# Kernel optimization log

Measured on AMD Instinct MI355X. Metric: run time of the kernel, lower is better.

The kernel has to match this reference:

```python
import jax, jax.numpy as jnp
import numpy as np

N_EXPERTS = 32
NUM_EXP = 4  # 1 shared + 3 routed

def setup_inputs() -> dict:
    key = jax.random.key(0)
    ks = jax.random.split(key, 4)
    b, t, c, h = 2, 2048, 256, 1024
    x = jax.random.normal(ks[0], (b, t, c), dtype=jnp.float32)
    gate_W = jax.random.normal(ks[1], (c, N_EXPERTS - 1), dtype=jnp.float32) / np.sqrt(c)
    gate_b = jnp.zeros((N_EXPERTS - 1,), jnp.float32)
    expert_bias = jnp.zeros((N_EXPERTS - 1,), jnp.float32)
    W1 = jax.random.normal(ks[2], (N_EXPERTS, c, h), dtype=jnp.float32) / np.sqrt(c)
    b1 = jnp.zeros((N_EXPERTS, h), jnp.float32)
    W2 = jax.random.normal(ks[3], (N_EXPERTS, h, c), dtype=jnp.float32) / np.sqrt(h)
    b2 = jnp.zeros((N_EXPERTS, c), jnp.float32)
    return {"x": x, "gate_W": gate_W, "gate_b": gate_b, "expert_bias": expert_bias,
            "W1": W1, "b1": b1, "W2": W2, "b2": b2}

def reference(x, gate_W, gate_b, expert_bias, W1, b1, W2, b2):
    # Eval mode: dropout and UnitCenteredNoise are identity.
    b, t, c = x.shape
    xf = x.reshape(b * t, c)                       # [N, c]
    N = xf.shape[0]

    # --- Router: softmax gate over 31 routed experts, bias, top-(num_exp-1) ---
    gate_cont = jax.nn.softmax(xf @ gate_W + gate_b, axis=-1)   # [N, 31]
    biased = gate_cont + expert_bias
    vals, idx = jax.lax.top_k(biased, NUM_EXP - 1)              # [N, 3]
    vals = vals / jnp.sum(vals, axis=-1, keepdims=True)
    shared_w = jnp.full((N, 1), 1.0 / NUM_EXP, dtype=x.dtype)
    gate_vals = jnp.concatenate([shared_w, vals * (NUM_EXP - 1) / NUM_EXP], axis=-1)  # [N, 4]
    idx_full = jnp.concatenate([jnp.zeros_like(idx[:, :1]), idx + 1], axis=-1)        # [N, 4]

    # --- Dense compute of ALL experts (faithful to original) ---
    hid = jax.nn.gelu(jnp.einsum('nc,ech->enh', xf, W1) + b1[:, None, :])  # [E, N, h]
    expert_out = jnp.einsum('enh,ehc->enc', hid, W2) + b2[:, None, :]      # [E, N, c]

    # --- Scatter gate weights into dense [N, E] router matrix ---
    router_weights = jnp.zeros((N, N_EXPERTS), dtype=x.dtype)
    router_weights = router_weights.at[jnp.arange(N)[:, None], idx_full].add(gate_vals)

    # --- Masked weighted sum over experts ---
    out = jnp.einsum('enc,ne->nc', expert_out, router_weights)  # [N, c]
    return out.reshape(b, t, c), router_weights
```

## Files before the change

### kernel.cpp

```cpp
#include <hip/hip_runtime.h>
#include <hip/hip_bf16.h>

#define NTOK 4096
#define CDIM 256
#define HDIM 1024
#define NEXP 32
#define MT   64
#define LDX  264
#define TP   72
#define NCPY 8
#define SEG  512
#define DUMP 16384
#define SROWS (DUMP + 1)

typedef __bf16 bf16x8 __attribute__((ext_vector_type(8)));
typedef float  f32x4  __attribute__((ext_vector_type(4)));

__device__ __forceinline__ unsigned short f2bf(float f) {
    __hip_bfloat16 h = __float2bfloat16(f);
    return __builtin_bit_cast(unsigned short, h);
}

__device__ __forceinline__ float gelu_fast(float v) {
    float c = 0.7978845608028654f * (v + 0.044715f * v * v * v);
    return v * __builtin_amdgcn_rcpf(1.f + __expf(-2.f * c));
}

__launch_bounds__(256, 4)
__global__ void k_prep(const float* __restrict__ x, const float* __restrict__ gW,
                       const float* __restrict__ gb, const float* __restrict__ eb,
                       const float* __restrict__ W1, const float* __restrict__ W2,
                       float* __restrict__ rw, unsigned short* __restrict__ xb,
                       int* __restrict__ cnt8, int* __restrict__ list, float* __restrict__ w4,
                       unsigned short* __restrict__ W1s, unsigned short* __restrict__ W2s)
{
    __shared__ __align__(16) unsigned char SMEM[4 * 32 * TP * 2];
    const int bx = blockIdx.x, tid = threadIdx.x;
    const int l = tid & 63, q = l >> 4, m16 = l & 15;

    if (bx < 1024) {
        float* xs = (float*)SMEM;
        const int wv = tid >> 6;
        const int n = bx * 4 + wv;
        const float* xr = x + (size_t)n * CDIM;
        float4 v = *(const float4*)(xr + l * 4);
        ushort4 u; u.x = f2bf(v.x); u.y = f2bf(v.y); u.z = f2bf(v.z); u.w = f2bf(v.w);
        *(ushort4*)(xb + (size_t)n * CDIM + l * 4) = u;
        *(float4*)(&xs[wv * 256 + l * 4]) = v;
        __syncthreads();

        float logit = -1e30f;
        if (l < 31) {
            float acc = 0.f;
            #pragma unroll 8
            for (int k = 0; k < CDIM; ++k) acc = fmaf(xs[wv * 256 + k], gW[k * 31 + l], acc);
            logit = acc + gb[l];
        }
        float mx = logit;
        #pragma unroll
        for (int o = 32; o; o >>= 1) mx = fmaxf(mx, __shfl_xor(mx, o));
        float p = (l < 31) ? expf(logit - mx) : 0.f;
        float s = p;
        #pragma unroll
        for (int o = 32; o; o >>= 1) s += __shfl_xor(s, o);
        float bv = (l < 31) ? p / s + eb[l] : -1e30f;
        float tv[3]; int ti[3];
        #pragma unroll
        for (int r = 0; r < 3; ++r) {
            float m = bv;
            #pragma unroll
            for (int o = 32; o; o >>= 1) m = fmaxf(m, __shfl_xor(m, o));
            unsigned long long msk = __ballot(bv == m);
            int src = __ffsll(msk) - 1;
            tv[r] = m; ti[r] = src;
            if (l == src) bv = -1e30f;
        }
        float invs = 0.75f / (tv[0] + tv[1] + tv[2]);
        float w0 = tv[0] * invs, w1 = tv[1] * invs, w2 = tv[2] * invs;
        if (l < 32) {
            float val = (l == 0) ? 0.25f : 0.f;
            if (l == ti[0] + 1) val = w0;
            if (l == ti[1] + 1) val = w1;
            if (l == ti[2] + 1) val = w2;
            rw[(size_t)n * NEXP + l] = val;
        }
        if (l == 0) {
            w4[n*4+0] = 0.25f; w4[n*4+1] = w0; w4[n*4+2] = w1; w4[n*4+3] = w2;
            const int c = bx & (NCPY - 1);
            #pragma unroll
            for (int sslot = 1; sslot <= 3; ++sslot) {
                int e = ti[sslot - 1] + 1;
                int pos = atomicAdd(&cnt8[((e - 1) * NCPY + c) * 32], 1);
                list[e * NTOK + c * SEG + pos] = n * 4 + sslot;
            }
        }
    } else {
        const int w = tid >> 6;
        const int st = (bx - 1024) * 4 + w;
        unsigned short* T = (unsigned short*)SMEM + w * 32 * TP;

        const float* src; int ld; int e, kb, sn; bool isW1;
        if (st < 4096) {
            isW1 = true;
            e = st >> 7; int rem = st & 127; kb = rem >> 4; sn = rem & 15;
            src = W1 + ((size_t)(e * CDIM + kb * 32)) * HDIM + sn * 64; ld = HDIM;
        } else {
            isW1 = false;
            int s2 = st - 4096;
            e = s2 >> 7; int rem = s2 & 127; kb = rem >> 2; sn = rem & 3;
            src = W2 + ((size_t)(e * HDIM + kb * 32)) * CDIM + sn * 64; ld = CDIM;
        }
        const int rr = l >> 4, cc = (l & 15) * 4;
        #pragma unroll
        for (int i = 0; i < 8; ++i) {
            float4 v = *(const float4*)(src + (size_t)(i * 4 + rr) * ld + cc);
            ushort4 u; u.x = f2bf(v.x); u.y = f2bf(v.y); u.z = f2bf(v.z); u.w = f2bf(v.w);
            *(ushort4*)(T + (i * 4 + rr) * TP + cc) = u;
        }
        __syncthreads();
        #pragma unroll
        for (int nb2 = 0; nb2 < 4; ++nb2) {
            unsigned short t[8];
            #pragma unroll
            for (int j = 0; j < 8; ++j) t[j] = T[(q * 8 + j) * TP + nb2 * 16 + m16];
            uint4 u;
            u.x = (unsigned)t[0] | ((unsigned)t[1] << 16);
            u.y = (unsigned)t[2] | ((unsigned)t[3] << 16);
            u.z = (unsigned)t[4] | ((unsigned)t[5] << 16);
            u.w = (unsigned)t[6] | ((unsigned)t[7] << 16);
            if (isW1) {
                size_t gw = (size_t)e * 512 + (sn * 4 + nb2) * 8 + kb;
                *(uint4*)(W1s + gw * 512 + l * 8) = u;
            } else {
                size_t g2 = (size_t)e * 512 + (sn * 4 + nb2) * 32 + kb;
                *(uint4*)(W2s + g2 * 512 + l * 8) = u;
            }
        }
    }
}

__launch_bounds__(256, 2)
__global__ void k_moe(const unsigned short* __restrict__ xb,
                      const unsigned short* __restrict__ W1s,
                      const float* __restrict__ b1,
                      const unsigned short* __restrict__ W2s,
                      const float* __restrict__ b2,
                      const int* __restrict__ cnt8, const int* __restrict__ list,
                      const float* __restrict__ w4, float* __restrict__ scratch)
{
    __shared__ __align__(16) unsigned short Xb[MT * LDX];
    __shared__ __align__(16) unsigned short Hb[MT * LDX];
    __shared__ float wgts[MT];
    __shared__ int   srow[MT];
    __shared__ int   pref[NEXP + 1];
    __shared__ int   cnts[NEXP];
    __shared__ int   cpre[NEXP - 1][NCPY + 1];

    const int tid = threadIdx.x, w = tid >> 6, l = tid & 63, q = l >> 4, m16 = l & 15;

    if (tid < NEXP - 1) {
        int a = 0;
        cpre[tid][0] = 0;
        #pragma unroll
        for (int c = 0; c < NCPY; ++c) {
            a += cnt8[(tid * NCPY + c) * 32];
            cpre[tid][c + 1] = a;
        }
        cnts[tid + 1] = a;
    }
    if (tid == NEXP - 1) cnts[0] = NTOK;
    __syncthreads();
    if (tid == 0) {
        int a = 0;
        for (int e = 0; e < NEXP; ++e) { pref[e] = a; a += (cnts[e] + MT - 1) >> 6; }
        pref[NEXP] = a;
    }
    __syncthreads();
    const int nitems = pref[NEXP] * 2;

    const f32x4 fzero = {0.f, 0.f, 0.f, 0.f};

    for (int it = blockIdx.x; it < nitems; it += gridDim.x) {
        const int c2 = it & 1, t = it >> 1;
        int e = 0;
        while (pref[e + 1] <= t) ++e;
        const int tile = t - pref[e];
        const int nvalid = min(MT, cnts[e] - tile * MT);
        const int nc0 = c2 * 2;

        const unsigned short* w1n = W1s + ((size_t)(e * 64 + nc0 * 16 + 4 * w) * 8) * 512 + l * 8;
        bf16x8 wb[3][4];
        #pragma unroll
        for (int k = 0; k < 3; ++k)
            #pragma unroll
            for (int bj = 0; bj < 4; ++bj)
                wb[k][bj] = *(const bf16x8*)(w1n + bj * 4096 + k * 512);

        __syncthreads();

        if (tid < MT) {
            float wv = 0.f; int sa = DUMP;
            if (tid < nvalid) {
                int pp = tile * MT + tid, a;
                if (e == 0) a = pp << 2;
                else {
                    int c = 0;
                    while (cpre[e - 1][c + 1] <= pp) ++c;
                    a = list[e * NTOK + c * SEG + (pp - cpre[e - 1][c])];
                }
                sa = a; wv = w4[a];
            }
            srow[tid] = sa; wgts[tid] = wv;
        }
        {
            const int xrow = tid >> 2, seg = (tid & 3) * 64;
            int a = 0;
            if (xrow < nvalid) {
                int pp = tile * MT + xrow;
                if (e == 0) a = pp << 2;
                else {
                    int c = 0;
                    while (cpre[e - 1][c + 1] <= pp) ++c;
                    a = list[e * NTOK + c * SEG + (pp - cpre[e - 1][c])];
                }
            }
            const unsigned short* xr = xb + (size_t)(a >> 2) * CDIM + seg;
            unsigned short* dst = Xb + xrow * LDX + seg;
            #pragma unroll
            for (int j = 0; j < 64; j += 8)
                *(uint4*)(dst + j) = *(const uint4*)(xr + j);
        }
        __syncthreads();

        f32x4 acc[4][4];
        #pragma unroll
        for (int i = 0; i < 4; ++i)
            #pragma unroll
            for (int j = 0; j < 4; ++j) acc[i][j] = fzero;

        #pragma unroll
        for (int hc = 0; hc < 2; ++hc) {
            const int nc = nc0 + hc;
            const unsigned short* w1c = W1s + ((size_t)(e * 64 + nc * 16 + 4 * w) * 8) * 512 + l * 8;
            const unsigned short* w2c = W2s + ((size_t)(e * 16 + 4 * w) * 32 + nc * 8) * 512 + l * 8;

            f32x4 hacc[4][4];
            #pragma unroll
            for (int i = 0; i < 4; ++i)
                #pragma unroll
                for (int j = 0; j < 4; ++j) hacc[i][j] = fzero;

            #pragma unroll
            for (int ks = 0; ks < 8; ++ks) {
                bf16x8 af[4];
                #pragma unroll
                for (int ai = 0; ai < 4; ++ai)
                    af[ai] = *(const bf16x8*)(Xb + (16*ai + m16) * LDX + ks*32 + q*8);
                #pragma unroll
                for (int ai = 0; ai < 4; ++ai)
                    #pragma unroll
                    for (int bj = 0; bj < 4; ++bj)
                        hacc[ai][bj] = __builtin_amdgcn_mfma_f32_16x16x32_bf16(af[ai], wb[ks % 3][bj], hacc[ai][bj], 0, 0, 0);
                if (ks < 5) {
                    #pragma unroll
                    for (int bj = 0; bj < 4; ++bj)
                        wb[ks % 3][bj] = *(const bf16x8*)(w1c + bj * 4096 + (ks + 3) * 512);
                }
            }
            #pragma unroll
            for (int k = 0; k < 3; ++k)
                #pragma unroll
                for (int bj = 0; bj < 4; ++bj)
                    wb[k][bj] = *(const bf16x8*)(w2c + bj * 16384 + k * 512);

            #pragma unroll
            for (int bj = 0; bj < 4; ++bj) {
                int colc = 64*w + 16*bj + m16;
                float bv = b1[e * HDIM + nc * 256 + colc];
                #pragma unroll
                for (int ai = 0; ai < 4; ++ai)
                    #pragma unroll
                    for (int r = 0; r < 4; ++r) {
                        int row = 16*ai + 4*q + r;
                        Hb[row * LDX + colc] = f2bf(gelu_fast(hacc[ai][bj][r] + bv));
                    }
            }
            __syncthreads();

            #pragma unroll
            for (int ks = 0; ks < 8; ++ks) {
                bf16x8 af[4];
                #pragma unroll
                for (int ai = 0; ai < 4; ++ai)
                    af[ai] = *(const bf16x8*)(Hb + (16*ai + m16) * LDX + ks*32 + q*8);
                #pragma unroll
                for (int ai = 0; ai < 4; ++ai)
                    #pragma unroll
                    for (int bj = 0; bj < 4; ++bj)
                        acc[ai][bj] = __builtin_amdgcn_mfma_f32_16x16x32_bf16(af[ai], wb[ks % 3][bj], acc[ai][bj], 0, 0, 0);
                if (ks < 5) {
                    #pragma unroll
                    for (int bj = 0; bj < 4; ++bj)
                        wb[ks % 3][bj] = *(const bf16x8*)(w2c + bj * 16384 + (ks + 3) * 512);
                }
            }
            if (hc == 0) {
                const unsigned short* w1x = W1s + ((size_t)(e * 64 + (nc0 + 1) * 16 + 4 * w) * 8) * 512 + l * 8;
                #pragma unroll
                for (int k = 0; k < 3; ++k)
                    #pragma unroll
                    for (int bj = 0; bj < 4; ++bj)
                        wb[k][bj] = *(const bf16x8*)(w1x + bj * 4096 + k * 512);
            }
            __syncthreads();
        }

        #pragma unroll
        for (int bj = 0; bj < 4; ++bj) {
            int col = 64*w + 16*bj + m16;
            float b2v = (c2 == 0) ? b2[e * CDIM + col] : 0.f;
            #pragma unroll
            for (int ai = 0; ai < 4; ++ai)
                #pragma unroll
                for (int r = 0; r < 4; ++r) {
                    int row = 16*ai + 4*q + r;
                    float v = (acc[ai][bj][r] + b2v) * wgts[row];
                    scratch[((size_t)c2 * SROWS + srow[row]) * 256 + col] = v;
                }
        }
    }
}

__global__ void k_reduce(const float* __restrict__ scratch, float* __restrict__ out)
{
    const int gid = blockIdx.x * 256 + threadIdx.x;
    const int n = gid >> 6, c4 = (gid & 63) * 4;
    const float* s0 = scratch + ((size_t)n * 4) * 256 + c4;
    const float* s1 = scratch + ((size_t)SROWS + (size_t)n * 4) * 256 + c4;
    f32x4 acc = *(const f32x4*)(s0);
    acc += *(const f32x4*)(s0 + 256);
    acc += *(const f32x4*)(s0 + 512);
    acc += *(const f32x4*)(s0 + 768);
    acc += *(const f32x4*)(s1);
    acc += *(const f32x4*)(s1 + 256);
    acc += *(const f32x4*)(s1 + 512);
    acc += *(const f32x4*)(s1 + 768);
    *(f32x4*)(out + (size_t)n * CDIM + c4) = acc;
}

extern "C" void kernel_launch(void* const* d_in, const int* in_sizes, int n_in,
                              void* d_out, int out_size, void* d_ws, size_t ws_size,
                              hipStream_t stream)
{
    const float* x  = (const float*)d_in[0];
    const float* gW = (const float*)d_in[1];
    const float* gb = (const float*)d_in[2];
    const float* eb = (const float*)d_in[3];
    const float* W1 = (const float*)d_in[4];
    const float* b1 = (const float*)d_in[5];
    const float* W2 = (const float*)d_in[6];
    const float* b2 = (const float*)d_in[7];
    float* out = (float*)d_out;
    float* rw  = out + (size_t)NTOK * CDIM;

    char* p = (char*)d_ws;
    int*   cnt8 = (int*)p;
    float* w4   = (float*)(p + 32768);
    int*   list = (int*)(p + 32768 + 65536);
    unsigned short* xbuf = (unsigned short*)(p + (1 << 20));
    unsigned short* W1s  = xbuf + (size_t)NTOK * CDIM;
    unsigned short* W2s  = W1s + (size_t)NEXP * CDIM * HDIM;
    float* scratch = (float*)(p + ((size_t)40 << 20));

    hipMemsetAsync(cnt8, 0, 32768, stream);

    k_prep<<<3072, 256, 0, stream>>>(x, gW, gb, eb, W1, W2,
                                     rw, xbuf, cnt8, list, w4, W1s, W2s);
    k_moe<<<512, 256, 0, stream>>>(xbuf, W1s, b1, W2s, b2, cnt8, list, w4, scratch);
    k_reduce<<<1024, 256, 0, stream>>>(scratch, out);
}
```

Before: 178.5 us.

## Double token tile to 128 and share one LDS buffer for X and hidden

Raises the per-item token tile from 64 to 128 and swaps the MFMA operands so weights are the A operand and tokens the B operand. Each weight fragment is then reused across eight token blocks. The separate X and H LDS buffers are merged into one. Because X is overwritten by the hidden activations, it is reloaded from global memory after the first hidden chunk. Output is accumulated per chunk with a read-modify-write of the scratch buffer instead of being kept in registers across both chunks. The aim is to halve weight traffic per token, at the cost of higher register pressure, fewer work items for load balancing, extra scratch traffic and an extra X reload.

```diff
diff --git a/kernel.cpp b/kernel.cpp
--- a/kernel.cpp
+++ b/kernel.cpp
@@ -5,7 +5,7 @@
 #define CDIM 256
 #define HDIM 1024
 #define NEXP 32
-#define MT   64
+#define MT   128
 #define LDX  264
 #define TP   72
 #define NCPY 8
@@ -148,8 +148,7 @@
                       const int* __restrict__ cnt8, const int* __restrict__ list,
                       const float* __restrict__ w4, float* __restrict__ scratch)
 {
-    __shared__ __align__(16) unsigned short Xb[MT * LDX];
-    __shared__ __align__(16) unsigned short Hb[MT * LDX];
+    __shared__ __align__(16) unsigned short XH[MT * LDX];
     __shared__ float wgts[MT];
     __shared__ int   srow[MT];
     __shared__ int   pref[NEXP + 1];
@@ -172,7 +171,7 @@
     __syncthreads();
     if (tid == 0) {
         int a = 0;
-        for (int e = 0; e < NEXP; ++e) { pref[e] = a; a += (cnts[e] + MT - 1) >> 6; }
+        for (int e = 0; e < NEXP; ++e) { pref[e] = a; a += (cnts[e] + MT - 1) >> 7; }
         pref[NEXP] = a;
     }
     __syncthreads();
@@ -193,8 +192,8 @@
         #pragma unroll
         for (int k = 0; k < 3; ++k)
             #pragma unroll
-            for (int bj = 0; bj < 4; ++bj)
-                wb[k][bj] = *(const bf16x8*)(w1n + bj * 4096 + k * 512);
+            for (int hj = 0; hj < 4; ++hj)
+                wb[k][hj] = *(const bf16x8*)(w1n + hj * 4096 + k * 512);
 
         __syncthreads();
 
@@ -213,7 +212,7 @@
             srow[tid] = sa; wgts[tid] = wv;
         }
         {
-            const int xrow = tid >> 2, seg = (tid & 3) * 64;
+            const int xrow = tid >> 1, seg = (tid & 1) * 128;
             int a = 0;
             if (xrow < nvalid) {
                 int pp = tile * MT + xrow;
@@ -225,83 +224,87 @@
                 }
             }
             const unsigned short* xr = xb + (size_t)(a >> 2) * CDIM + seg;
-            unsigned short* dst = Xb + xrow * LDX + seg;
-            #pragma unroll
-            for (int j = 0; j < 64; j += 8)
+            unsigned short* dst = XH + xrow * LDX + seg;
+            #pragma unroll
+            for (int j = 0; j < 128; j += 8)
                 *(uint4*)(dst + j) = *(const uint4*)(xr + j);
         }
         __syncthreads();
 
-        f32x4 acc[4][4];
-        #pragma unroll
-        for (int i = 0; i < 4; ++i)
-            #pragma unroll
-            for (int j = 0; j < 4; ++j) acc[i][j] = fzero;
-
-        #pragma unroll
+        f32x4 acc[4][8];
+
+        #pragma unroll 1
         for (int hc = 0; hc < 2; ++hc) {
             const int nc = nc0 + hc;
             const unsigned short* w1c = W1s + ((size_t)(e * 64 + nc * 16 + 4 * w) * 8) * 512 + l * 8;
             const unsigned short* w2c = W2s + ((size_t)(e * 16 + 4 * w) * 32 + nc * 8) * 512 + l * 8;
 
-            f32x4 hacc[4][4];
             #pragma unroll
             for (int i = 0; i < 4; ++i)
                 #pragma unroll
-                for (int j = 0; j < 4; ++j) hacc[i][j] = fzero;
+                for (int j = 0; j < 8; ++j) acc[i][j] = fzero;
 
             #pragma unroll
             for (int ks = 0; ks < 8; ++ks) {
-                bf16x8 af[4];
-                #pragma unroll
-                for (int ai = 0; ai < 4; ++ai)
-                    af[ai] = *(const bf16x8*)(Xb + (16*ai + m16) * LDX + ks*32 + q*8);
-                #pragma unroll
-                for (int ai = 0; ai < 4; ++ai)
-                    #pragma unroll
-                    for (int bj = 0; bj < 4; ++bj)
-                        hacc[ai][bj] = __builtin_amdgcn_mfma_f32_16x16x32_bf16(af[ai], wb[ks % 3][bj], hacc[ai][bj], 0, 0, 0);
+                bf16x8 xf[8];
+                #pragma unroll
+                for (int tk = 0; tk < 8; ++tk)
+                    xf[tk] = *(const bf16x8*)(XH + (16*tk + m16) * LDX + ks*32 + q*8);
+                #pragma unroll
+                for (int hj = 0; hj < 4; ++hj)
+                    #pragma unroll
+                    for (int tk = 0; tk < 8; ++tk)
+                        acc[hj][tk] = __builtin_amdgcn_mfma_f32_16x16x32_bf16(wb[ks % 3][hj], xf[tk], acc[hj][tk], 0, 0, 0);
                 if (ks < 5) {
                     #pragma unroll
-                    for (int bj = 0; bj < 4; ++bj)
-                        wb[ks % 3][bj] = *(const bf16x8*)(w1c + bj * 4096 + (ks + 3) * 512);
+                    for (int hj = 0; hj < 4; ++hj)
+                        wb[ks % 3][hj] = *(const bf16x8*)(w1c + hj * 4096 + (ks + 3) * 512);
                 }
             }
             #pragma unroll
             for (int k = 0; k < 3; ++k)
                 #pragma unroll
-                for (int bj = 0; bj < 4; ++bj)
-                    wb[k][bj] = *(const bf16x8*)(w2c + bj * 16384 + k * 512);
-
-            #pragma unroll
-            for (int bj = 0; bj < 4; ++bj) {
-                int colc = 64*w + 16*bj + m16;
-                float bv = b1[e * HDIM + nc * 256 + colc];
-                #pragma unroll
-                for (int ai = 0; ai < 4; ++ai)
-                    #pragma unroll
-                    for (int r = 0; r < 4; ++r) {
-                        int row = 16*ai + 4*q + r;
-                        Hb[row * LDX + colc] = f2bf(gelu_fast(hacc[ai][bj][r] + bv));
-                    }
-            }
+                for (int cj = 0; cj < 4; ++cj)
+                    wb[k][cj] = *(const bf16x8*)(w2c + cj * 16384 + k * 512);
+
             __syncthreads();
 
             #pragma unroll
+            for (int hj = 0; hj < 4; ++hj) {
+                const int hid0 = 64*w + 16*hj + 4*q;
+                const float4 b1v = *(const float4*)(b1 + e * HDIM + nc * 256 + hid0);
+                #pragma unroll
+                for (int tk = 0; tk < 8; ++tk) {
+                    ushort4 hv;
+                    hv.x = f2bf(gelu_fast(acc[hj][tk][0] + b1v.x));
+                    hv.y = f2bf(gelu_fast(acc[hj][tk][1] + b1v.y));
+                    hv.z = f2bf(gelu_fast(acc[hj][tk][2] + b1v.z));
+                    hv.w = f2bf(gelu_fast(acc[hj][tk][3] + b1v.w));
+                    *(ushort4*)(XH + (16*tk + m16) * LDX + hid0) = hv;
+                }
+            }
+            __syncthreads();
+
+            #pragma unroll
+            for (int i = 0; i < 4; ++i)
+                #pragma unroll
+                for (int j = 0; j < 8; ++j) acc[i][j] = fzero;
+
+            #pragma unroll
             for (int ks = 0; ks < 8; ++ks) {
-                bf16x8 af[4];
-                #pragma unroll
-                for (int ai = 0; ai < 4; ++ai)
-                    af[ai] = *(const bf16x8*)(Hb + (16*ai + m16) * LDX + ks*32 + q*8);
-                #pragma unroll
-                for (int ai = 0; ai < 4; ++ai)
-                    #pragma unroll
-                    for (int bj = 0; bj < 4; ++bj)
-                        acc[ai][bj] = __builtin_amdgcn_mfma_f32_16x16x32_bf16(af[ai], wb[ks % 3][bj], acc[ai][bj], 0, 0, 0);
+                bf16x8 hf[8];
+                #pragma unroll
+                for (int tk = 0; tk < 8; ++tk)
+                    hf[tk] = *(const bf16x8*)(XH + (16*tk + m16) * LDX + ks*32 + q*8);
+                #pragma unroll
+                for (int cj = 0; cj < 4; ++cj)
+                    #pragma unroll
+                    for (int tk = 0; tk < 8; ++tk)
+                        acc[cj][tk] = __builtin_amdgcn_mfma_f32_16x16x32_bf16(wb[ks % 3][cj], hf[tk], acc[cj][tk], 0, 0, 0);
                 if (ks < 5) {
                     #pragma unroll
-                    for (int bj = 0; bj < 4; ++bj)
-                        wb[ks % 3][bj] = *(const bf16x8*)(w2c + bj * 16384 + (ks + 3) * 512);
+                    for (int cj = 0; cj < 4; ++cj)
+                        wb[ks % 3][cj] = *(const bf16x8*)(w2c + cj * 16384 + (ks + 3) * 512);
                 }
             }
             if (hc == 0) {
@@ -309,24 +312,39 @@
                 #pragma unroll
                 for (int k = 0; k < 3; ++k)
                     #pragma unroll
-                    for (int bj = 0; bj < 4; ++bj)
-                        wb[k][bj] = *(const bf16x8*)(w1x + bj * 4096 + k * 512);
+                    for (int hj = 0; hj < 4; ++hj)
+                        wb[k][hj] = *(const bf16x8*)(w1x + hj * 4096 + k * 512);
+            }
+
+            #pragma unroll
+            for (int cj = 0; cj < 4; ++cj) {
+                const int col0 = 64*w + 16*cj + 4*q;
+                float4 b2v = {0.f, 0.f, 0.f, 0.f};
+                if (c2 == 0 && hc == 1) b2v = *(const float4*)(b2 + e * CDIM + col0);
+                #pragma unroll
+                for (int tk = 0; tk < 8; ++tk) {
+                    const int tok = 16*tk + m16;
+                    const float wv = wgts[tok];
+                    float* sp = scratch + ((size_t)c2 * SROWS + srow[tok]) * 256 + col0;
+                    f32x4 v;
+                    v[0] = (acc[cj][tk][0] + b2v.x) * wv;
+                    v[1] = (acc[cj][tk][1] + b2v.y) * wv;
+                    v[2] = (acc[cj][tk][2] + b2v.z) * wv;
+                    v[3] = (acc[cj][tk][3] + b2v.w) * wv;
+                    if (hc == 1) v += *(const f32x4*)sp;
+                    *(f32x4*)sp = v;
+                }
             }
             __syncthreads();
-        }
-
-        #pragma unroll
-        for (int bj = 0; bj < 4; ++bj) {
-            int col = 64*w + 16*bj + m16;
-            float b2v = (c2 == 0) ? b2[e * CDIM + col] : 0.f;
-            #pragma unroll
-            for (int ai = 0; ai < 4; ++ai)
-                #pragma unroll
-                for (int r = 0; r < 4; ++r) {
-                    int row = 16*ai + 4*q + r;
-                    float v = (acc[ai][bj][r] + b2v) * wgts[row];
-                    scratch[((size_t)c2 * SROWS + srow[row]) * 256 + col] = v;
-                }
+            if (hc == 0) {
+                const int xrow = tid >> 1, seg = (tid & 1) * 128;
+                const unsigned short* xr = xb + (size_t)(srow[xrow] >= DUMP ? 0 : (srow[xrow] >> 2)) * CDIM + seg;
+                unsigned short* dst = XH + xrow * LDX + seg;
+                #pragma unroll
+                for (int j = 0; j < 128; j += 8)
+                    *(uint4*)(dst + j) = *(const uint4*)(xr + j);
+                __syncthreads();
+            }
         }
     }
 }
```

Measured after the change: 222.2 us. +24.5%, slower.
